# Kernel optimization log

Measured on AMD Instinct MI355X. Metric: run time of the kernel, lower is better.

The kernel has to match this reference:

```python
import jax, jax.numpy as jnp
import numpy as np

EPS = 1e-15
PROJ_EPS = 4e-3  # float32 boundary eps (geoopt convention)

def _artanh(x):
    return jnp.arctanh(jnp.clip(x, -1.0 + 1e-7, 1.0 - 1e-7))

def _norm(x, axis=-1):
    return jnp.maximum(jnp.sqrt(jnp.sum(x * x, axis=axis, keepdims=True)), EPS)

def expmap0(u, c):
    sc = jnp.sqrt(c)
    n = _norm(u)
    return jnp.tanh(sc * n) * u / (sc * n)

def project(x, c):
    n = _norm(x)
    maxn = (1.0 - PROJ_EPS) / jnp.sqrt(c)
    return jnp.where(n > maxn, x / n * maxn, x)

def mobius_pointwise_mul(w, x, c):
    sc = jnp.sqrt(c)
    wx = w * x
    xn = _norm(x)
    wxn = _norm(wx)
    return jnp.tanh(wxn / xn * _artanh(sc * xn)) * wx / (wxn * sc)

def mobius_add(x, y, c):
    x2 = jnp.sum(x * x, -1, keepdims=True)
    y2 = jnp.sum(y * y, -1, keepdims=True)
    xy = jnp.sum(x * y, -1, keepdims=True)
    num = (1.0 + 2.0 * c * xy + c * y2) * x + (1.0 - c * x2) * y
    den = 1.0 + 2.0 * c * xy + (c ** 2) * x2 * y2
    return num / jnp.maximum(den, EPS)

def logmap0(y, c):
    sc = jnp.sqrt(c)
    n = _norm(y)
    return _artanh(sc * n) * y / (sc * n)

def weighted_midpoint_batched(mix, c):
    # mix: (B, D, L); feature axis = 1 (torch call: dim=0 per sample), reduce over L.
    lam = 2.0 / jnp.maximum(1.0 - c * jnp.sum(mix * mix, axis=1, keepdims=True), EPS)  # (B,1,L)
    nom = jnp.sum(lam * mix, axis=2)          # (B, D)
    den = jnp.sum(lam - 1.0, axis=2)          # (B, 1)
    den = jnp.where(den >= 0, jnp.maximum(den, 1e-10), jnp.minimum(den, -1e-10))
    tm = nom / den                            # (B, D) "two_mean"
    # mobius_scalar_mul(0.5, tm)
    sc = jnp.sqrt(c)
    n = _norm(tm)
    return jnp.tanh(0.5 * _artanh(sc * n)) * tm / (sc * n)

def setup_inputs() -> dict:
    key = jax.random.key(0)
    ks = jax.random.split(key, 7)
    B, O, L, D = 64, 1, 1024, 1024
    return {
        "query": jax.random.normal(ks[0], (B, O, D), jnp.float32),
        "context": jax.random.normal(ks[1], (B, L, D), jnp.float32),
        "delta_t": jax.random.uniform(ks[2], (B, 1, L), jnp.float32),
        "c": jnp.ones((1,), jnp.float32),
        "W_in": jax.random.normal(ks[3], (D, D), jnp.float32) / np.float32(np.sqrt(D)),
        "W_out": jax.random.normal(ks[4], (D, 2 * D), jnp.float32) / np.float32(np.sqrt(2 * D)),
        "ae": jax.random.normal(ks[5], (B, 1, 1), jnp.float32) * 0.1,
        "ab": jax.random.normal(ks[6], (B, 1, 1), jnp.float32) * 0.1,
    }

def reference(query, context, delta_t, c, W_in, W_out, ae, ab):
    # linear_in (attention_type='general'): no bias
    q = jnp.einsum('bod,ed->boe', query, W_in)                     # (B,O,D)
    scores = jnp.einsum('bod,bld->bol', q, context)                # (B,O,L)
    aw = jax.nn.softmax(scores, axis=-1)
    aw = project(expmap0(aw, c), c)                                # hyperbolic attn weights
    ctx_t = jnp.transpose(context, (0, 2, 1))                      # (B,D,L)
    mix = project(mobius_pointwise_mul(aw, ctx_t, c), c)           # (B,D,L)
    bt = jnp.exp(-ab * delta_t)                                    # (B,1,L)
    bt = project(expmap0(bt, c), c)
    tmp = project(mobius_pointwise_mul(ae, mix, c), c)
    tmp = project(mobius_pointwise_mul(tmp, bt, c), c)
    term2 = jax.nn.relu(tmp)
    mix = project(mobius_add(mix, term2, c), c)
    fin = weighted_midpoint_batched(mix, c)[:, None, :]            # (B,1,D)
    mixl = logmap0(fin, c)
    combined = jnp.concatenate([mixl, q], axis=-1)                 # (B,1,2D)
    out = jnp.tanh(jnp.einsum('boe,de->bod', combined, W_out))     # (B,1,D)
    return (out, aw)
```

## Files before the change

### kernel.cpp

```cpp
#include <hip/hip_runtime.h>
#include <math.h>

#define BB 64
#define LL 1024
#define DD 1024

__device__ __forceinline__ float artanh_c(float x){
  x = fminf(fmaxf(x, -1.f + 1e-7f), 1.f - 1e-7f);
  return 0.5f * __logf((1.f + x) / (1.f - x));
}

__device__ __forceinline__ float wave_sum(float v){
  #pragma unroll
  for(int o = 32; o > 0; o >>= 1) v += __shfl_down(v, o, 64);
  return v;
}

__device__ __forceinline__ float block_sum(float v, float* red){
  v = wave_sum(v);
  int wid = threadIdx.x >> 6, lane = threadIdx.x & 63;
  __syncthreads();
  if(lane == 0) red[wid] = v;
  __syncthreads();
  if(wid == 0){
    float t = lane < 16 ? red[lane] : 0.f;
    #pragma unroll
    for(int o = 8; o > 0; o >>= 1) t += __shfl_down(t, o, 64);
    if(lane == 0) red[0] = t;
  }
  __syncthreads();
  return red[0];
}

__device__ __forceinline__ float block_max(float v, float* red){
  #pragma unroll
  for(int o = 32; o > 0; o >>= 1) v = fmaxf(v, __shfl_down(v, o, 64));
  int wid = threadIdx.x >> 6, lane = threadIdx.x & 63;
  __syncthreads();
  if(lane == 0) red[wid] = v;
  __syncthreads();
  if(wid == 0){
    float t = lane < 16 ? red[lane] : -INFINITY;
    #pragma unroll
    for(int o = 8; o > 0; o >>= 1) t = fmaxf(t, __shfl_down(t, o, 64));
    if(lane == 0) red[0] = t;
  }
  __syncthreads();
  return red[0];
}

__global__ void k_qproj(const float* __restrict__ query, const float* __restrict__ Win,
                        float* __restrict__ q){
  int wave = threadIdx.x >> 6, lane = threadIdx.x & 63;
  int e = blockIdx.x * 4 + wave;
  int b0 = blockIdx.y * 16;
  const float4* Wr = (const float4*)(Win + (size_t)e * DD);
  float4 w[4];
  #pragma unroll
  for(int j = 0; j < 4; j++) w[j] = Wr[j * 64 + lane];
  for(int bb = 0; bb < 16; bb++){
    int b = b0 + bb;
    const float4* qr = (const float4*)(query + (size_t)b * DD);
    float acc = 0.f;
    #pragma unroll
    for(int j = 0; j < 4; j++){
      float4 v = qr[j * 64 + lane];
      acc += w[j].x * v.x + w[j].y * v.y + w[j].z * v.z + w[j].w * v.w;
    }
    acc = wave_sum(acc);
    if(lane == 0) q[b * DD + e] = acc;
  }
}

__global__ void k_scores(const float* __restrict__ qv, const float* __restrict__ ctx,
                         float* __restrict__ scores){
  int b = blockIdx.y;
  int wave = threadIdx.x >> 6, lane = threadIdx.x & 63;
  int l = blockIdx.x * 4 + wave;
  __shared__ float4 qs4[DD / 4];
  if(threadIdx.x < 256) qs4[threadIdx.x] = ((const float4*)(qv + (size_t)b * DD))[threadIdx.x];
  __syncthreads();
  const float4* cr = (const float4*)(ctx + ((size_t)b * LL + l) * DD);
  float acc = 0.f;
  #pragma unroll
  for(int it = 0; it < 4; it++){
    int idx = it * 64 + lane;
    float4 v = cr[idx];
    float4 qq = qs4[idx];
    acc += qq.x * v.x + qq.y * v.y + qq.z * v.z + qq.w * v.w;
  }
  acc = wave_sum(acc);
  if(lane == 0) scores[b * LL + l] = acc;
}

__global__ void k_softmax_tr(const float* __restrict__ scores, const float* __restrict__ dt,
                             const float* __restrict__ ab, const float* __restrict__ cp,
                             float* __restrict__ awt, float* __restrict__ aw_out,
                             float* __restrict__ btt, float* __restrict__ btn){
  __shared__ float red[16];
  int b = blockIdx.x, tid = threadIdx.x;
  float c = cp[0], sc = sqrtf(c), maxn = (1.f - 4e-3f) / sc;
  float s = scores[b * LL + tid];
  float m = block_max(s, red);
  float e = __expf(s - m);
  float Z = block_sum(e, red);
  float aw = e / Z;
  float S = block_sum(aw * aw, red);
  float n = fmaxf(sqrtf(S), 1e-15f);
  float tau = tanhf(sc * n) / (sc * n);
  float n1 = fmaxf(tau * sqrtf(S), 1e-15f);
  float s1 = n1 > maxn ? maxn / n1 : 1.f;
  float awf = tau * s1 * aw;
  awt[b * LL + tid] = awf;
  aw_out[b * LL + tid] = awf;
  float btv = __expf(-ab[b] * dt[b * LL + tid]);
  float S2 = block_sum(btv * btv, red);
  float n2 = fmaxf(sqrtf(S2), 1e-15f);
  float tau2 = tanhf(sc * n2) / (sc * n2);
  float nb = fmaxf(tau2 * sqrtf(S2), 1e-15f);
  float s2 = nb > maxn ? maxn / nb : 1.f;
  float btf = tau2 * s2 * btv;
  btt[b * LL + tid] = btf;
  if(tid == 0) btn[b] = fmaxf(tau2 * s2 * sqrtf(S2), 1e-15f);
}

__global__ void k_stats(const float* __restrict__ ctx, const float* __restrict__ awt,
                        const float* __restrict__ btt, float* __restrict__ stats){
  int tid = threadIdx.x;
  int b = blockIdx.x;
  int l0 = blockIdx.y * 128;
  __shared__ float ws_[128], bs_[128];
  if(tid < 128){ ws_[tid] = awt[b * LL + l0 + tid]; bs_[tid] = btt[b * LL + l0 + tid]; }
  __syncthreads();
  const float4* cpx = (const float4*)(ctx + ((size_t)b * LL + l0) * DD) + tid;
  float r2[4] = {0,0,0,0}, p2[4] = {0,0,0,0};
  float s3p[4] = {0,0,0,0}, s3m[4] = {0,0,0,0};
  float s5p[4] = {0,0,0,0}, s5m[4] = {0,0,0,0};
  #pragma unroll 4
  for(int i = 0; i < 128; i++){
    float4 rv = cpx[(size_t)i * (DD / 4)];
    float w = ws_[i], bt = bs_[i];
    float rr[4] = {rv.x, rv.y, rv.z, rv.w};
    #pragma unroll
    for(int c = 0; c < 4; c++){
      float r = rr[c];
      float p = w * r;
      r2[c] = fmaf(r, r, r2[c]);
      p2[c] = fmaf(p, p, p2[c]);
      float pb = p * bt;
      float pb2 = pb * pb;
      float p2bt = (p * p) * bt;
      if(r > 0.f){ s3p[c] += pb2; s5p[c] += p2bt; } else { s3m[c] += pb2; s5m[c] += p2bt; }
    }
  }
  int d = tid * 4;
  float* base = stats + (size_t)b * 6 * DD + d;
  #pragma unroll
  for(int c = 0; c < 4; c++){
    atomicAdd(base + 0 * DD + c, r2[c]);
    atomicAdd(base + 1 * DD + c, p2[c]);
    atomicAdd(base + 2 * DD + c, s3p[c]);
    atomicAdd(base + 3 * DD + c, s3m[c]);
    atomicAdd(base + 4 * DD + c, s5p[c]);
    atomicAdd(base + 5 * DD + c, s5m[c]);
  }
}

__global__ void k_finish(const float* __restrict__ stats, const float* __restrict__ ae,
                         const float* __restrict__ btn, const float* __restrict__ cp,
                         float* __restrict__ rowsc){
  int row = blockIdx.x * 256 + threadIdx.x;
  int b = row >> 10;
  int d = row & (DD - 1);
  float c = cp[0], sc = sqrtf(c), maxn = (1.f - 4e-3f) / sc;
  const float* st = stats + (size_t)b * 6 * DD + d;
  float r2 = st[0], p2 = st[DD], s3p = st[2 * DD], s3m = st[3 * DD], s5p = st[4 * DD], s5m = st[5 * DD];
  float sp2 = sqrtf(p2);
  float xn  = fmaxf(sqrtf(r2), 1e-15f);
  float wxn = fmaxf(sp2, 1e-15f);
  float at1 = artanh_c(sc * xn);
  float alpha = tanhf(wxn / xn * at1) / (wxn * sc);
  float n1 = fmaxf(alpha * sp2, 1e-15f);
  float beta = alpha * (n1 > maxn ? maxn / n1 : 1.f);
  float aeb = ae[b];
  float mixn_raw = beta * sp2;
  float xn2  = fmaxf(mixn_raw, 1e-15f);
  float wxn2 = fmaxf(fabsf(aeb) * mixn_raw, 1e-15f);
  float at2 = artanh_c(sc * xn2);
  float coef_t = tanhf(wxn2 / xn2 * at2) * aeb * beta / (wxn2 * sc);
  float n2 = fmaxf(fabsf(coef_t) * sp2, 1e-15f);
  float g = coef_t * (n2 > maxn ? maxn / n2 : 1.f);
  float s3 = s3p + s3m;
  float sq3 = sqrtf(s3);
  float xn3 = btn[b];
  float wxn3 = fmaxf(fabsf(g) * sq3, 1e-15f);
  float at3 = artanh_c(sc * xn3);
  float coef2 = tanhf(wxn3 / xn3 * at3) * g / (wxn3 * sc);
  float n3 = fmaxf(fabsf(coef2) * sq3, 1e-15f);
  float k = coef2 * (n3 > maxn ? maxn / n3 : 1.f);
  bool kp = k > 0.f;
  float ssel  = kp ? s3p : s3m;
  float s5sel = kp ? s5p : s5m;
  float y2 = k * k * ssel;
  float xy = beta * k * s5sel;
  float x2 = beta * beta * p2;
  float A  = 1.f + 2.f * c * xy + c * y2;
  float Bc = 1.f - c * x2;
  float den = 1.f + 2.f * c * xy + c * c * x2 * y2;
  den = fmaxf(den, 1e-15f);
  float U0 = A * beta / den;
  float V0 = Bc * k / den;
  float nf2 = U0 * U0 * p2 + 2.f * U0 * V0 * s5sel + V0 * V0 * ssel;
  float nf = fmaxf(sqrtf(nf2), 1e-15f);
  float s4 = nf > maxn ? maxn / nf : 1.f;
  float U = U0 * s4, V = V0 * s4;
  float4* out4 = (float4*)(rowsc + (size_t)row * 4);
  *out4 = make_float4(U, kp ? V : 0.f, kp ? 0.f : V, 0.f);
}

__global__ void k_colsum(const float* __restrict__ ctx, const float* __restrict__ awt,
                         const float* __restrict__ btt, const float* __restrict__ rowsc,
                         float* __restrict__ colsum){
  int b = blockIdx.y;
  int l0 = blockIdx.x * 16;
  int wave = threadIdx.x >> 6, lane = threadIdx.x & 63;
  float U[4][4], Vp[4][4], Vm[4][4];
  const float4* rp = (const float4*)rowsc + (size_t)b * DD;
  #pragma unroll
  for(int it = 0; it < 4; it++){
    int d4 = it * 64 + lane;
    #pragma unroll
    for(int j = 0; j < 4; j++){
      float4 t = rp[d4 * 4 + j];
      U[it][j] = t.x; Vp[it][j] = t.y; Vm[it][j] = t.z;
    }
  }
  const float4* cb = (const float4*)(ctx + (size_t)b * LL * DD);
  for(int row = wave; row < 16; row += 4){
    int l = l0 + row;
    float w = awt[b * LL + l], bt = btt[b * LL + l];
    float acc = 0.f;
    #pragma unroll
    for(int it = 0; it < 4; it++){
      float4 rv = cb[(size_t)l * (DD / 4) + it * 64 + lane];
      float rr[4] = {rv.x, rv.y, rv.z, rv.w};
      #pragma unroll
      for(int c = 0; c < 4; c++){
        float r = rr[c];
        float p = w * r;
        float t = r > 0.f ? Vp[it][c] : Vm[it][c];
        float mv = p * (U[it][c] + bt * t);
        acc = fmaf(mv, mv, acc);
      }
    }
    acc = wave_sum(acc);
    if(lane == 0) colsum[b * LL + l] = acc;
  }
}

__global__ void k_lam(const float* __restrict__ colsum, const float* __restrict__ cp,
                      float* __restrict__ lam, float* __restrict__ denw){
  __shared__ float red[16];
  int b = blockIdx.x, tid = threadIdx.x;
  float c = cp[0];
  float csv = colsum[b * LL + tid];
  float lv = 2.f / fmaxf(1.f - c * csv, 1e-15f);
  lam[b * LL + tid] = lv;
  float dsum = block_sum(lv - 1.f, red);
  if(tid == 0){
    denw[b] = dsum >= 0.f ? fmaxf(dsum, 1e-10f) : fminf(dsum, -1e-10f);
  }
}

__global__ void k_nom(const float* __restrict__ ctx, const float* __restrict__ awt,
                      const float* __restrict__ btt, const float* __restrict__ lam,
                      const float* __restrict__ rowsc, float* __restrict__ nom){
  int tid = threadIdx.x;
  int b = blockIdx.x;
  int l0 = blockIdx.y * 128;
  __shared__ float ws_[128], bs_[128], ls_[128];
  if(tid < 128){
    ws_[tid] = awt[b * LL + l0 + tid];
    bs_[tid] = btt[b * LL + l0 + tid];
    ls_[tid] = lam[b * LL + l0 + tid];
  }
  __syncthreads();
  float U[4], Vp[4], Vm[4];
  const float4* rp = (const float4*)rowsc + (size_t)b * DD + tid * 4;
  #pragma unroll
  for(int j = 0; j < 4; j++){ float4 t = rp[j]; U[j] = t.x; Vp[j] = t.y; Vm[j] = t.z; }
  const float4* cpx = (const float4*)(ctx + ((size_t)b * LL + l0) * DD) + tid;
  float acc[4] = {0,0,0,0};
  #pragma unroll 4
  for(int i = 0; i < 128; i++){
    float4 rv = cpx[(size_t)i * (DD / 4)];
    float w = ws_[i], bt = bs_[i], lv = ls_[i];
    float rr[4] = {rv.x, rv.y, rv.z, rv.w};
    #pragma unroll
    for(int c = 0; c < 4; c++){
      float r = rr[c];
      float p = w * r;
      float t = r > 0.f ? Vp[c] : Vm[c];
      float mv = p * (U[c] + bt * t);
      acc[c] = fmaf(lv, mv, acc[c]);
    }
  }
  #pragma unroll
  for(int c = 0; c < 4; c++) atomicAdd(nom + (size_t)b * DD + tid * 4 + c, acc[c]);
}

__global__ void k_mid(const float* __restrict__ nom, const float* __restrict__ denw,
                      const float* __restrict__ qv, const float* __restrict__ cp,
                      float* __restrict__ comb){
  __shared__ float red[16];
  int b = blockIdx.x, tid = threadIdx.x;
  float c = cp[0], sc = sqrtf(c);
  float tm = nom[b * DD + tid] / denw[b];
  float S = block_sum(tm * tm, red);
  float n = fmaxf(sqrtf(S), 1e-15f);
  float at = artanh_c(sc * n);
  float mu = tanhf(0.5f * at) / (sc * n);
  float n2 = fmaxf(mu * sqrtf(S), 1e-15f);
  float nu = artanh_c(sc * n2) / (sc * n2);
  comb[b * 2 * DD + tid] = nu * mu * tm;
  comb[b * 2 * DD + DD + tid] = qv[b * DD + tid];
}

__global__ void k_out(const float* __restrict__ comb, const float* __restrict__ Wout,
                      float* __restrict__ outp){
  int wave = threadIdx.x >> 6, lane = threadIdx.x & 63;
  int d = blockIdx.x * 4 + wave;
  int b0 = blockIdx.y * 16;
  const float4* Wr = (const float4*)(Wout + (size_t)d * 2 * DD);
  float4 w[8];
  #pragma unroll
  for(int j = 0; j < 8; j++) w[j] = Wr[j * 64 + lane];
  for(int bb = 0; bb < 16; bb++){
    int b = b0 + bb;
    const float4* cb = (const float4*)(comb + (size_t)b * 2 * DD);
    float acc = 0.f;
    #pragma unroll
    for(int j = 0; j < 8; j++){
      float4 v = cb[j * 64 + lane];
      acc += w[j].x * v.x + w[j].y * v.y + w[j].z * v.z + w[j].w * v.w;
    }
    acc = wave_sum(acc);
    if(lane == 0) outp[b * DD + d] = tanhf(acc);
  }
}

extern "C" void kernel_launch(void* const* d_in, const int* in_sizes, int n_in,
                              void* d_out, int out_size, void* d_ws, size_t ws_size,
                              hipStream_t stream) {
  const float* query = (const float*)d_in[0];
  const float* ctx   = (const float*)d_in[1];
  const float* dt    = (const float*)d_in[2];
  const float* cp    = (const float*)d_in[3];
  const float* Win   = (const float*)d_in[4];
  const float* Wout  = (const float*)d_in[5];
  const float* ae    = (const float*)d_in[6];
  const float* ab    = (const float*)d_in[7];
  float* out = (float*)d_out;
  float* ws  = (float*)d_ws;

  float* q_      = ws;
  float* awt_    = ws + 65536;
  float* btt_    = ws + 131072;
  float* btn_    = ws + 196608;
  float* den_    = ws + 196672;
  float* scores_ = ws + 196736;
  float* stats_  = ws + 262272;
  float* nom_    = ws + 655488;
  float* rowsc_  = ws + 721024;
  float* colsum_ = ws + 983168;
  float* lam_  = scores_;
  float* comb_ = stats_;

  hipMemsetAsync(stats_, 0, (size_t)(393216 + 65536) * sizeof(float), stream);

  k_qproj     <<<dim3(256, 4),  256,  0, stream>>>(query, Win, q_);
  k_scores    <<<dim3(256, BB), 256,  0, stream>>>(q_, ctx, scores_);
  k_softmax_tr<<<BB,            1024, 0, stream>>>(scores_, dt, ab, cp, awt_, out + BB * DD, btt_, btn_);
  k_stats     <<<dim3(BB, 8),   256,  0, stream>>>(ctx, awt_, btt_, stats_);
  k_finish    <<<256,           256,  0, stream>>>(stats_, ae, btn_, cp, rowsc_);
  k_colsum    <<<dim3(64, BB),  256,  0, stream>>>(ctx, awt_, btt_, rowsc_, colsum_);
  k_lam       <<<BB,            1024, 0, stream>>>(colsum_, cp, lam_, den_);
  k_nom       <<<dim3(BB, 8),   256,  0, stream>>>(ctx, awt_, btt_, lam_, rowsc_, nom_);
  k_mid       <<<BB,            1024, 0, stream>>>(nom_, den_, q_, cp, comb_);
  k_out       <<<dim3(256, 4),  256,  0, stream>>>(comb_, Wout, out);
}
```

Baseline: 615.0 us.

## Fuse colsum, lambda and nominator passes into one LDS-staged context kernel

Merges k_colsum, k_lam and k_nom into one kernel, k_mixagg. Each block stages 16 context rows (64KB) in shared memory, computes the per-row squared norms and lambda values, then accumulates the lambda-weighted nominator from the same staged tile. This removes one full read of the 256MB context tensor and two kernel launches. The lambda-sum denominator moves into k_mid. k_stats also gets a finer split over L (64 rows per block, twice as many blocks) to raise parallelism, at the cost of twice as many atomic adds per output. The 64KB shared allocation limits occupancy to a few blocks per CU.

```diff
diff --git a/kernel.cpp b/kernel.cpp
--- a/kernel.cpp
+++ b/kernel.cpp
@@ -128,16 +128,16 @@
                         const float* __restrict__ btt, float* __restrict__ stats){
   int tid = threadIdx.x;
   int b = blockIdx.x;
-  int l0 = blockIdx.y * 128;
-  __shared__ float ws_[128], bs_[128];
-  if(tid < 128){ ws_[tid] = awt[b * LL + l0 + tid]; bs_[tid] = btt[b * LL + l0 + tid]; }
+  int l0 = blockIdx.y * 64;
+  __shared__ float ws_[64], bs_[64];
+  if(tid < 64){ ws_[tid] = awt[b * LL + l0 + tid]; bs_[tid] = btt[b * LL + l0 + tid]; }
   __syncthreads();
   const float4* cpx = (const float4*)(ctx + ((size_t)b * LL + l0) * DD) + tid;
   float r2[4] = {0,0,0,0}, p2[4] = {0,0,0,0};
   float s3p[4] = {0,0,0,0}, s3m[4] = {0,0,0,0};
   float s5p[4] = {0,0,0,0}, s5m[4] = {0,0,0,0};
   #pragma unroll 4
-  for(int i = 0; i < 128; i++){
+  for(int i = 0; i < 64; i++){
     float4 rv = cpx[(size_t)i * (DD / 4)];
     float w = ws_[i], bt = bs_[i];
     float rr[4] = {rv.x, rv.y, rv.z, rv.w};
@@ -218,13 +218,21 @@
   *out4 = make_float4(U, kp ? V : 0.f, kp ? 0.f : V, 0.f);
 }
 
-__global__ void k_colsum(const float* __restrict__ ctx, const float* __restrict__ awt,
-                         const float* __restrict__ btt, const float* __restrict__ rowsc,
-                         float* __restrict__ colsum){
+__global__ __launch_bounds__(256) void k_mixagg(const float* __restrict__ ctx,
+                         const float* __restrict__ awt, const float* __restrict__ btt,
+                         const float* __restrict__ rowsc, const float* __restrict__ cp,
+                         float* __restrict__ lam_out, float* __restrict__ nom){
+  __shared__ float4 cs4[16 * 256];
+  __shared__ float aw_s[16], bt_s[16], lam_s[16];
   int b = blockIdx.y;
   int l0 = blockIdx.x * 16;
-  int wave = threadIdx.x >> 6, lane = threadIdx.x & 63;
-  float U[4][4], Vp[4][4], Vm[4][4];
+  int tid = threadIdx.x, wave = tid >> 6, lane = tid & 63;
+  float c = cp[0];
+  const float4* cg = (const float4*)(ctx + ((size_t)b * LL + l0) * DD);
+  #pragma unroll
+  for(int r = 0; r < 16; r++) cs4[r * 256 + tid] = cg[r * 256 + tid];
+  if(tid < 16){ aw_s[tid] = awt[b * LL + l0 + tid]; bt_s[tid] = btt[b * LL + l0 + tid]; }
+  float U1[4][4], Vp1[4][4], Vm1[4][4];
   const float4* rp = (const float4*)rowsc + (size_t)b * DD;
   #pragma unroll
   for(int it = 0; it < 4; it++){
@@ -232,90 +240,71 @@
     #pragma unroll
     for(int j = 0; j < 4; j++){
       float4 t = rp[d4 * 4 + j];
-      U[it][j] = t.x; Vp[it][j] = t.y; Vm[it][j] = t.z;
-    }
-  }
-  const float4* cb = (const float4*)(ctx + (size_t)b * LL * DD);
-  for(int row = wave; row < 16; row += 4){
-    int l = l0 + row;
-    float w = awt[b * LL + l], bt = btt[b * LL + l];
+      U1[it][j] = t.x; Vp1[it][j] = t.y; Vm1[it][j] = t.z;
+    }
+  }
+  float U2[4], Vp2[4], Vm2[4];
+  #pragma unroll
+  for(int j = 0; j < 4; j++){
+    float4 t = rp[tid * 4 + j];
+    U2[j] = t.x; Vp2[j] = t.y; Vm2[j] = t.z;
+  }
+  __syncthreads();
+  #pragma unroll
+  for(int rr = 0; rr < 4; rr++){
+    int r = wave + rr * 4;
+    float w = aw_s[r], bt = bt_s[r];
     float acc = 0.f;
     #pragma unroll
     for(int it = 0; it < 4; it++){
-      float4 rv = cb[(size_t)l * (DD / 4) + it * 64 + lane];
-      float rr[4] = {rv.x, rv.y, rv.z, rv.w};
+      float4 rv = cs4[r * 256 + it * 64 + lane];
+      float rx[4] = {rv.x, rv.y, rv.z, rv.w};
       #pragma unroll
-      for(int c = 0; c < 4; c++){
-        float r = rr[c];
-        float p = w * r;
-        float t = r > 0.f ? Vp[it][c] : Vm[it][c];
-        float mv = p * (U[it][c] + bt * t);
+      for(int j = 0; j < 4; j++){
+        float rc = rx[j];
+        float p = w * rc;
+        float t = rc > 0.f ? Vp1[it][j] : Vm1[it][j];
+        float mv = p * (U1[it][j] + bt * t);
         acc = fmaf(mv, mv, acc);
       }
     }
     acc = wave_sum(acc);
-    if(lane == 0) colsum[b * LL + l] = acc;
-  }
-}
-
-__global__ void k_lam(const float* __restrict__ colsum, const float* __restrict__ cp,
-                      float* __restrict__ lam, float* __restrict__ denw){
-  __shared__ float red[16];
-  int b = blockIdx.x, tid = threadIdx.x;
-  float c = cp[0];
-  float csv = colsum[b * LL + tid];
-  float lv = 2.f / fmaxf(1.f - c * csv, 1e-15f);
-  lam[b * LL + tid] = lv;
-  float dsum = block_sum(lv - 1.f, red);
-  if(tid == 0){
-    denw[b] = dsum >= 0.f ? fmaxf(dsum, 1e-10f) : fminf(dsum, -1e-10f);
-  }
-}
-
-__global__ void k_nom(const float* __restrict__ ctx, const float* __restrict__ awt,
-                      const float* __restrict__ btt, const float* __restrict__ lam,
-                      const float* __restrict__ rowsc, float* __restrict__ nom){
-  int tid = threadIdx.x;
-  int b = blockIdx.x;
-  int l0 = blockIdx.y * 128;
-  __shared__ float ws_[128], bs_[128], ls_[128];
-  if(tid < 128){
-    ws_[tid] = awt[b * LL + l0 + tid];
-    bs_[tid] = btt[b * LL + l0 + tid];
-    ls_[tid] = lam[b * LL + l0 + tid];
-  }
-  __syncthreads();
-  float U[4], Vp[4], Vm[4];
-  const float4* rp = (const float4*)rowsc + (size_t)b * DD + tid * 4;
-  #pragma unroll
-  for(int j = 0; j < 4; j++){ float4 t = rp[j]; U[j] = t.x; Vp[j] = t.y; Vm[j] = t.z; }
-  const float4* cpx = (const float4*)(ctx + ((size_t)b * LL + l0) * DD) + tid;
-  float acc[4] = {0,0,0,0};
+    if(lane == 0){
+      float lv = 2.f / fmaxf(1.f - c * acc, 1e-15f);
+      lam_s[r] = lv;
+      lam_out[b * LL + l0 + r] = lv;
+    }
+  }
+  __syncthreads();
+  float acc2[4] = {0, 0, 0, 0};
   #pragma unroll 4
-  for(int i = 0; i < 128; i++){
-    float4 rv = cpx[(size_t)i * (DD / 4)];
-    float w = ws_[i], bt = bs_[i], lv = ls_[i];
-    float rr[4] = {rv.x, rv.y, rv.z, rv.w};
-    #pragma unroll
-    for(int c = 0; c < 4; c++){
-      float r = rr[c];
-      float p = w * r;
-      float t = r > 0.f ? Vp[c] : Vm[c];
-      float mv = p * (U[c] + bt * t);
-      acc[c] = fmaf(lv, mv, acc[c]);
-    }
-  }
-  #pragma unroll
-  for(int c = 0; c < 4; c++) atomicAdd(nom + (size_t)b * DD + tid * 4 + c, acc[c]);
-}
-
-__global__ void k_mid(const float* __restrict__ nom, const float* __restrict__ denw,
+  for(int r = 0; r < 16; r++){
+    float w = aw_s[r], bt = bt_s[r], lv = lam_s[r];
+    float4 rv = cs4[r * 256 + tid];
+    float rx[4] = {rv.x, rv.y, rv.z, rv.w};
+    #pragma unroll
+    for(int j = 0; j < 4; j++){
+      float rc = rx[j];
+      float p = w * rc;
+      float t = rc > 0.f ? Vp2[j] : Vm2[j];
+      float mv = p * (U2[j] + bt * t);
+      acc2[j] = fmaf(lv, mv, acc2[j]);
+    }
+  }
+  #pragma unroll
+  for(int j = 0; j < 4; j++) atomicAdd(nom + (size_t)b * DD + tid * 4 + j, acc2[j]);
+}
+
+__global__ void k_mid(const float* __restrict__ nom, const float* __restrict__ lam,
                       const float* __restrict__ qv, const float* __restrict__ cp,
                       float* __restrict__ comb){
   __shared__ float red[16];
   int b = blockIdx.x, tid = threadIdx.x;
   float c = cp[0], sc = sqrtf(c);
-  float tm = nom[b * DD + tid] / denw[b];
+  float lv = lam[b * LL + tid];
+  float dsum = block_sum(lv - 1.f, red);
+  float den = dsum >= 0.f ? fmaxf(dsum, 1e-10f) : fminf(dsum, -1e-10f);
+  float tm = nom[b * DD + tid] / den;
   float S = block_sum(tm * tm, red);
   float n = fmaxf(sqrtf(S), 1e-15f);
   float at = artanh_c(sc * n);
@@ -367,12 +356,10 @@
   float* awt_    = ws + 65536;
   float* btt_    = ws + 131072;
   float* btn_    = ws + 196608;
-  float* den_    = ws + 196672;
-  float* scores_ = ws + 196736;
-  float* stats_  = ws + 262272;
-  float* nom_    = ws + 655488;
-  float* rowsc_  = ws + 721024;
-  float* colsum_ = ws + 983168;
+  float* scores_ = ws + 196672;
+  float* stats_  = ws + 262208;
+  float* nom_    = ws + 655424;
+  float* rowsc_  = ws + 720960;
   float* lam_  = scores_;
   float* comb_ = stats_;
 
@@ -381,11 +368,9 @@
   k_qproj     <<<dim3(256, 4),  256,  0, stream>>>(query, Win, q_);
   k_scores    <<<dim3(256, BB), 256,  0, stream>>>(q_, ctx, scores_);
   k_softmax_tr<<<BB,            1024, 0, stream>>>(scores_, dt, ab, cp, awt_, out + BB * DD, btt_, btn_);
-  k_stats     <<<dim3(BB, 8),   256,  0, stream>>>(ctx, awt_, btt_, stats_);
+  k_stats     <<<dim3(BB, 16),  256,  0, stream>>>(ctx, awt_, btt_, stats_);
   k_finish    <<<256,           256,  0, stream>>>(stats_, ae, btn_, cp, rowsc_);
-  k_colsum    <<<dim3(64, BB),  256,  0, stream>>>(ctx, awt_, btt_, rowsc_, colsum_);
-  k_lam       <<<BB,            1024, 0, stream>>>(colsum_, cp, lam_, den_);
-  k_nom       <<<dim3(BB, 8),   256,  0, stream>>>(ctx, awt_, btt_, lam_, rowsc_, nom_);
-  k_mid       <<<BB,            1024, 0, stream>>>(nom_, den_, q_, cp, comb_);
+  k_mixagg    <<<dim3(64, BB),  256,  0, stream>>>(ctx, awt_, btt_, rowsc_, cp, lam_, nom_);
+  k_mid       <<<BB,            1024, 0, stream>>>(nom_, lam_, q_, cp, comb_);
   k_out       <<<dim3(256, 4),  256,  0, stream>>>(comb_, Wout, out);
 }
```

Measured after the change: 635.2 us. 3.3% more time.
